# Optimization experiments

Hardware: AMD Instinct MI355X
Metric: run time of the kernel (lower is better)

## Reference

```python
import jax, jax.numpy as jnp
import numpy as np

N = 20000
F_IN = 500
HID = 64
CLS = 16
H = 4
K_KNN = 10
NEG_SLOPE = 0.2


def _edges(key, n_rand):
    # random edges plus self-loops (mirrors add_self_loops in the torch code)
    src = jax.random.randint(key, (n_rand,), 0, N)
    dst = jax.random.randint(jax.random.fold_in(key, 1), (n_rand,), 0, N)
    loops = jnp.arange(N)
    return jnp.stack([jnp.concatenate([src, loops]), jnp.concatenate([dst, loops])]).astype(jnp.int32)


def setup_inputs():
    key = jax.random.key(0)
    ks = jax.random.split(key, 40)
    inp = {}
    inp['x'] = jax.random.normal(ks[0], (N, F_IN), jnp.float32)
    inp['edge_index_1'] = _edges(ks[1], 16 * N)          # 1-hop graph, 340k edges
    inp['edge_index_2'] = _edges(ks[2], 32 * N)          # denser 2-hop graph, 660k edges
    knn_src = jnp.repeat(jnp.arange(N), K_KNN)
    knn_dst = jax.random.randint(ks[3], (K_KNN * N,), 0, N)
    inp['edge_index_knn'] = jnp.stack([knn_src, knn_dst]).astype(jnp.int32)

    def p(k, shape):
        return jax.random.normal(k, shape, jnp.float32) * 0.05

    dims = {1: (F_IN, HID), 2: (HID, CLS), 3: (F_IN, HID), 4: (HID, CLS), 5: (F_IN, HID), 6: (HID, CLS)}
    i = 4
    for j in range(1, 7):
        fi, fo = dims[j]
        inp[f'W{j}'] = p(ks[i], (fi, H, fo)); i += 1
        inp[f'as{j}'] = p(ks[i], (H, fo)); i += 1
        inp[f'ad{j}'] = p(ks[i], (H, fo)); i += 1
        inp[f'b{j}'] = jnp.zeros((fo,), jnp.float32)
    for j in range(1, 4):
        inp[f'lin{j}_w'] = p(ks[i], (CLS, CLS)); i += 1
        inp[f'lin{j}_b'] = jnp.zeros((CLS,), jnp.float32)
    inp['agg_w'] = p(ks[i], (CLS,))
    return inp


def gat_conv(x, ei, W, a_s, a_d, b):
    # PyG GATConv, concat=False (mean over heads). W: [F,H,D], a_s/a_d: [H,D], b: [D]
    src, dst = ei[0], ei[1]
    z = jnp.einsum('nf,fhd->nhd', x, W)                 # [N,H,D]
    e_src = jnp.sum(z * a_s, -1)                         # [N,H]
    e_dst = jnp.sum(z * a_d, -1)                         # [N,H]
    e = jax.nn.leaky_relu(e_src[src] + e_dst[dst], NEG_SLOPE)   # [E,H]
    m = jax.ops.segment_max(e, dst, num_segments=N)      # per-dst softmax (edge softmax)
    p = jnp.exp(e - m[dst])
    s = jax.ops.segment_sum(p, dst, num_segments=N)
    alpha = p / (s[dst] + 1e-16)                         # [E,H]
    out = jax.ops.segment_sum(alpha[:, :, None] * z[src], dst, num_segments=N)  # [N,H,D]
    return out.mean(1) + b


def reference(x, edge_index_1, edge_index_2, edge_index_knn,
              W1, as1, ad1, b1, W2, as2, ad2, b2,
              W3, as3, ad3, b3, W4, as4, ad4, b4,
              W5, as5, ad5, b5, W6, as6, ad6, b6,
              lin1_w, lin1_b, lin2_w, lin2_b, lin3_w, lin3_b, agg_w):
    # eval mode: dropout is a no-op
    h1 = jax.nn.relu(gat_conv(x, edge_index_1, W1, as1, ad1, b1))
    h1 = gat_conv(h1, edge_index_1, W2, as2, ad2, b2)
    h2 = jax.nn.relu(gat_conv(x, edge_index_2, W3, as3, ad3, b3))
    h2 = gat_conv(h2, edge_index_2, W4, as4, ad4, b4)
    h3 = jax.nn.relu(gat_conv(x, edge_index_knn, W5, as5, ad5, b5))
    h3 = gat_conv(h3, edge_index_knn, W6, as6, ad6, b6)

    a1 = jnp.tanh(h1 @ lin1_w + lin1_b) @ agg_w          # [N]
    a2 = jnp.tanh(h2 @ lin2_w + lin2_b) @ agg_w
    a3 = jnp.tanh(h3 @ lin3_w + lin3_b) @ agg_w
    a = jax.nn.softmax(jnp.stack([a1, a2, a3], axis=1), axis=1)  # [N,3]
    h = a[:, 0:1] * h1 + a[:, 1:2] * h2 + a[:, 2:3] * h3
    return jax.nn.log_softmax(h, axis=1)
```

## Files before the change

### kernel.cpp

```cpp
#include <hip/hip_runtime.h>
#include <hip/hip_bf16.h>
#include <math.h>

#define N_NODES 20000
#define MP      20096
#define FIN     500
#define KP      512
#define NBUCK   157

typedef unsigned short u16;
typedef unsigned char  u8;
typedef __attribute__((ext_vector_type(8))) short   short8;
typedef __attribute__((ext_vector_type(2))) unsigned uv2;
typedef __attribute__((ext_vector_type(2))) float   f32x2;
typedef __attribute__((ext_vector_type(4))) float   f32x4;

__device__ __forceinline__ float b2f(u16 u){
  union { unsigned int i; float f; } v; v.i = ((unsigned int)u) << 16; return v.f;
}
__device__ __forceinline__ u16 f2b(float f){
  __hip_bfloat16 h = __float2bfloat16(f);
  return *reinterpret_cast<u16*>(&h);
}
__device__ __forceinline__ float lrelu(float x){ return x >= 0.f ? x : 0.2f * x; }
__device__ __forceinline__ float ldp(const void* p, int i, int bf){
  return bf ? b2f(((const u16*)p)[i]) : ((const float*)p)[i];
}
__device__ __forceinline__ u8 f2fp8(float f){
  return (u8)(__builtin_amdgcn_cvt_pk_fp8_f32(f, 0.f, 0, false) & 0xff);
}
template<bool HI>
__device__ __forceinline__ f32x2 fp8pair(unsigned w){
  return __builtin_amdgcn_cvt_pk_f32_fp8((int)w, HI);
}
__device__ __forceinline__ void gll16(const u16* g, u16* l){
  __builtin_amdgcn_global_load_lds(
      (const __attribute__((address_space(1))) unsigned int*)g,
      (__attribute__((address_space(3))) unsigned int*)l, 16, 0, 0);
}

__global__ void detect_dtype_kernel(const unsigned int* __restrict__ xw, int nwords,
                                    int* __restrict__ flag){
  __shared__ int cnt;
  if (threadIdx.x == 0) cnt = 0;
  __syncthreads();
  int c = 0;
  for (int i = threadIdx.x; i < nwords; i += 256){
    unsigned e = (xw[i] >> 7) & 0xFF;
    if (e >= 0x70 && e <= 0x8F) c++;
  }
  atomicAdd(&cnt, c);
  __syncthreads();
  if (threadIdx.x == 0) *flag = (cnt * 2 > nwords) ? 1 : 0;
}

#define CHA 8192
__global__ __launch_bounds__(256) void prep_kernel(
    const void* __restrict__ x, u16* __restrict__ xp,
    const void* Wb0, const void* Wb1, const void* Wb2,
    const void* Ws0, const void* Ws1, const void* Ws2,
    u16* ob0, u16* ob1, u16* ob2, u16* os0, u16* os1, u16* os2,
    const int* s0, const int* s1, const int* s2,
    const int* d0, const int* d1, const int* d2,
    int E0, int E1, int E2, int S0, int S1, int S2, int EB,
    int* __restrict__ bucketCur, unsigned* p0, unsigned* p1, unsigned* p2,
    const int* __restrict__ flag){
  __shared__ int hb[NBUCK];
  __shared__ int hbase[NBUCK];
  int bf = *flag;
  if (blockIdx.y == 0){
    int t = blockIdx.x * 256 + threadIdx.x;
    if (t >= MP * 64) return;
    int row = t >> 6;
    int j0  = (t & 63) * 8;
    short8 v;
#pragma unroll
    for (int j = 0; j < 8; ++j){
      int k = j0 + j;
      u16 val = 0;
      if (row < N_NODES && k < FIN)
        val = bf ? ((const u16*)x)[(size_t)row * FIN + k]
                 : f2b(((const float*)x)[(size_t)row * FIN + k]);
      v[j] = (short)val;
    }
    *(short8*)(xp + (size_t)row * KP + j0) = v;
  } else if (blockIdx.y == 1){
    int xb = blockIdx.x;
    if (xb >= 6 * 512) return;
    int which = xb >> 9;
    int t = (xb & 511) * 256 + threadIdx.x;
    if (which < 3){
      if (t >= 256 * KP) return;
      const void* W = which == 0 ? Wb0 : (which == 1 ? Wb1 : Wb2);
      u16* O = which == 0 ? ob0 : (which == 1 ? ob1 : ob2);
      int n = t / KP, k = t % KP;
      u16 val = 0;
      if (k < FIN)
        val = bf ? ((const u16*)W)[(size_t)k * 256 + n]
                 : f2b(((const float*)W)[(size_t)k * 256 + n]);
      O[t] = val;
    } else {
      if (t >= 64 * 64) return;
      const void* W = which == 3 ? Ws0 : (which == 4 ? Ws1 : Ws2);
      u16* O = which == 3 ? os0 : (which == 4 ? os1 : os2);
      int n = t / 64, k = t % 64;
      O[t] = bf ? ((const u16*)W)[(size_t)k * 64 + n]
                : f2b(((const float*)W)[(size_t)k * 64 + n]);
    }
  } else {
    int sblk = blockIdx.x;
    if (sblk >= 3 * EB) return;
    int g = sblk / EB;
    const int* src = g == 0 ? s0 : (g == 1 ? s1 : s2);
    const int* dst = g == 0 ? d0 : (g == 1 ? d1 : d2);
    unsigned* pairs = g == 0 ? p0 : (g == 1 ? p1 : p2);
    int E = g == 0 ? E0 : (g == 1 ? E1 : E2);
    int S = g == 0 ? S0 : (g == 1 ? S1 : S2);
    int base = (sblk % EB) * CHA;
    if (base >= E) return;
    for (int i = threadIdx.x; i < NBUCK; i += 256) hb[i] = 0;
    __syncthreads();
    int rk[CHA / 256];
#pragma unroll
    for (int i = 0; i < CHA / 256; ++i){
      int e = base + i * 256 + threadIdx.x;
      rk[i] = 0;
      if (e < E) rk[i] = atomicAdd(&hb[dst[e] >> 7], 1);
    }
    __syncthreads();
    for (int i = threadIdx.x; i < NBUCK; i += 256)
      hbase[i] = atomicAdd(&bucketCur[g * NBUCK + i], hb[i]);
    __syncthreads();
#pragma unroll
    for (int i = 0; i < CHA / 256; ++i){
      int e = base + i * 256 + threadIdx.x;
      if (e < E){
        int d = dst[e];
        int b = d >> 7;
        int pos = hbase[b] + rk[i];
        if (pos < S)
          pairs[(size_t)b * S + pos] = ((unsigned)src[e] << 7) | (unsigned)(d & 127);
      }
    }
  }
}

__global__ __launch_bounds__(256) void csr_finalize_kernel(
    const unsigned* p0, const unsigned* p1, const unsigned* p2,
    int S0, int S1, int S2,
    const int* __restrict__ bucketCur,
    int* e0, int* e1, int* e2,
    int2* __restrict__ metaB){
  int g = blockIdx.y;
  const unsigned* pairs = g == 0 ? p0 : (g == 1 ? p1 : p2);
  int* esrc = g == 0 ? e0 : (g == 1 ? e1 : e2);
  int S = g == 0 ? S0 : (g == 1 ? S1 : S2);
  int2* meta = metaB + (size_t)g * MP;
  int b = blockIdx.x;
  int nb = bucketCur[g * NBUCK + b];
  if (nb > S) nb = S;
  const unsigned* pb = pairs + (size_t)b * S;
  int* eb = esrc + (size_t)b * S;
  __shared__ int cnt[128];
  __shared__ int loff[128];
  __shared__ int cur[128];
  if (threadIdx.x < 128) cnt[threadIdx.x] = 0;
  __syncthreads();
  for (int i = threadIdx.x; i < nb; i += 256)
    atomicAdd(&cnt[pb[i] & 127], 1);
  __syncthreads();
  if (threadIdx.x == 0){
    int run = 0;
    for (int k = 0; k < 128; ++k){ loff[k] = run; run += cnt[k]; }
  }
  __syncthreads();
  if (threadIdx.x < 128){
    cur[threadIdx.x] = loff[threadIdx.x];
    int d = b * 128 + threadIdx.x;
    if (d < N_NODES){
      int2 m; m.x = b * S + loff[threadIdx.x]; m.y = cnt[threadIdx.x];
      meta[d] = m;
    }
  }
  __syncthreads();
  for (int i = threadIdx.x; i < nb; i += 256){
    unsigned u = pb[i];
    int slot = atomicAdd(&cur[u & 127], 1);
    eb[slot] = (int)(u >> 7);
  }
}

__global__ __launch_bounds__(256) void gemm_big_kernel(const u16* __restrict__ A,
    const u16* B0, const u16* B1, const u16* B2,
    u8* C0, u8* C1, u8* C2,
    const void* as0, const void* as1, const void* as2,
    const void* ad0, const void* ad1, const void* ad2,
    float* __restrict__ esB, float* __restrict__ edB,
    const int* __restrict__ flag, int M){
  int g = blockIdx.z;
  const u16* BT = g == 0 ? B0 : (g == 1 ? B1 : B2);
  u8* C = g == 0 ? C0 : (g == 1 ? C1 : C2);
  const void* as_ = g == 0 ? as0 : (g == 1 ? as1 : as2);
  const void* ad_ = g == 0 ? ad0 : (g == 1 ? ad1 : ad2);
  float* es = esB + (size_t)g * N_NODES * 4;
  float* ed = edB + (size_t)g * N_NODES * 4;
  __shared__ alignas(16) u16 As[128 * 64];
  __shared__ alignas(16) u16 Bs[128 * 64];
  const int K = KP, Nn = 256;
  int t = threadIdx.x, lane = t & 63, w = t >> 6;
  int m0 = blockIdx.y * 128, n0 = blockIdx.x * 128;
  int mw = (w >> 1) * 64, nw = (w & 1) * 64;
  f32x4 acc[4][4] = {};
  for (int k0 = 0; k0 < K; k0 += 64){
    __syncthreads();
#pragma unroll
    for (int i = 0; i < 4; ++i){
      int c = i * 256 + w * 64 + lane;
      int row = c >> 3, kk = (c & 7) * 8;
      gll16(A  + (size_t)(m0 + row) * K + k0 + kk, As + (size_t)(i * 256 + w * 64) * 8);
      gll16(BT + (size_t)(n0 + row) * K + k0 + kk, Bs + (size_t)(i * 256 + w * 64) * 8);
    }
    __syncthreads();
#pragma unroll
    for (int ks = 0; ks < 2; ++ks){
      short8 af[4], bfr[4];
#pragma unroll
      for (int mi = 0; mi < 4; ++mi)
        af[mi] = *(const short8*)(As + (size_t)(mw + mi * 16 + (lane & 15)) * 64 + ks * 32 + (lane >> 4) * 8);
#pragma unroll
      for (int ni = 0; ni < 4; ++ni)
        bfr[ni] = *(const short8*)(Bs + (size_t)(nw + ni * 16 + (lane & 15)) * 64 + ks * 32 + (lane >> 4) * 8);
#pragma unroll
      for (int mi = 0; mi < 4; ++mi)
#pragma unroll
        for (int ni = 0; ni < 4; ++ni)
          acc[mi][ni] = __builtin_amdgcn_mfma_f32_16x16x32_bf16(af[mi], bfr[ni], acc[mi][ni], 0, 0, 0);
    }
  }
  int bf = *flag;
#pragma unroll
  for (int mi = 0; mi < 4; ++mi)
#pragma unroll
    for (int ni = 0; ni < 4; ++ni)
#pragma unroll
      for (int r = 0; r < 4; ++r){
        int row = m0 + mw + mi * 16 + (lane >> 4) * 4 + r;
        int col = n0 + nw + ni * 16 + (lane & 15);
        if (row < M) C[(size_t)row * Nn + col] = f2fp8(acc[mi][ni][r]);
      }
  {
    int h = (n0 + nw) >> 6;
    float asv[4], adv[4];
#pragma unroll
    for (int ni = 0; ni < 4; ++ni){
      int col = n0 + nw + ni * 16 + (lane & 15);
      asv[ni] = ldp(as_, col, bf);
      adv[ni] = ldp(ad_, col, bf);
    }
#pragma unroll
    for (int mi = 0; mi < 4; ++mi)
#pragma unroll
      for (int r = 0; r < 4; ++r){
        float ps = 0.f, pd2 = 0.f;
#pragma unroll
        for (int ni = 0; ni < 4; ++ni){
          ps  += acc[mi][ni][r] * asv[ni];
          pd2 += acc[mi][ni][r] * adv[ni];
        }
#pragma unroll
        for (int m2 = 1; m2 < 16; m2 <<= 1){
          ps  += __shfl_xor(ps, m2);
          pd2 += __shfl_xor(pd2, m2);
        }
        int row = m0 + mw + mi * 16 + (lane >> 4) * 4 + r;
        if ((lane & 15) == 0 && row < M){
          atomicAdd(es + (size_t)row * 4 + h, ps);
          atomicAdd(ed + (size_t)row * 4 + h, pd2);
        }
      }
  }
}

__global__ __launch_bounds__(256) void gemm_small_kernel(
    const u16* A0, const u16* A1, const u16* A2,
    const u16* B0, const u16* B1, const u16* B2,
    u8* C0, u8* C1, u8* C2,
    const void* as0, const void* as1, const void* as2,
    const void* ad0, const void* ad1, const void* ad2,
    float* __restrict__ esB, float* __restrict__ edB,
    const int* __restrict__ flag, int M){
  int g = blockIdx.y;
  const u16* A  = g == 0 ? A0 : (g == 1 ? A1 : A2);
  const u16* BT = g == 0 ? B0 : (g == 1 ? B1 : B2);
  u8* C = g == 0 ? C0 : (g == 1 ? C1 : C2);
  const void* as_ = g == 0 ? as0 : (g == 1 ? as1 : as2);
  const void* ad_ = g == 0 ? ad0 : (g == 1 ? ad1 : ad2);
  float* es = esB + (size_t)g * N_NODES * 4;
  float* ed = edB + (size_t)g * N_NODES * 4;
  __shared__ alignas(16) u16 As[64 * 64];
  __shared__ alignas(16) u16 Bs[64 * 64];
  int t = threadIdx.x, lane = t & 63, w = t >> 6;
  int m0 = blockIdx.x * 64;
#pragma unroll
  for (int i = 0; i < 2; ++i){
    int c = i * 256 + w * 64 + lane;
    int row = c >> 3, kk = (c & 7) * 8;
    gll16(A  + (size_t)(m0 + row) * 64 + kk, As + (size_t)(i * 256 + w * 64) * 8);
    gll16(BT + (size_t)row * 64 + kk,        Bs + (size_t)(i * 256 + w * 64) * 8);
  }
  __syncthreads();
  f32x4 acc[4] = {};
  int mw = w * 16;
#pragma unroll
  for (int ks = 0; ks < 2; ++ks){
    short8 af = *(const short8*)(As + (size_t)(mw + (lane & 15)) * 64 + ks * 32 + (lane >> 4) * 8);
#pragma unroll
    for (int ni = 0; ni < 4; ++ni){
      short8 bv = *(const short8*)(Bs + (size_t)(ni * 16 + (lane & 15)) * 64 + ks * 32 + (lane >> 4) * 8);
      acc[ni] = __builtin_amdgcn_mfma_f32_16x16x32_bf16(af, bv, acc[ni], 0, 0, 0);
    }
  }
  int bf = *flag;
#pragma unroll
  for (int ni = 0; ni < 4; ++ni)
#pragma unroll
    for (int r = 0; r < 4; ++r){
      int row = m0 + mw + (lane >> 4) * 4 + r;
      int col = ni * 16 + (lane & 15);
      if (row < M) C[(size_t)row * 64 + col] = f2fp8(acc[ni][r]);
    }
  {
    float asv[4], adv[4];
#pragma unroll
    for (int ni = 0; ni < 4; ++ni){
      int col = ni * 16 + (lane & 15);
      asv[ni] = ldp(as_, col, bf);
      adv[ni] = ldp(ad_, col, bf);
    }
#pragma unroll
    for (int r = 0; r < 4; ++r){
      float ps[4], pd2[4];
#pragma unroll
      for (int ni = 0; ni < 4; ++ni){ ps[ni] = acc[ni][r] * asv[ni]; pd2[ni] = acc[ni][r] * adv[ni]; }
#pragma unroll
      for (int m2 = 1; m2 < 16; m2 <<= 1)
#pragma unroll
        for (int ni = 0; ni < 4; ++ni){
          ps[ni]  += __shfl_xor(ps[ni], m2);
          pd2[ni] += __shfl_xor(pd2[ni], m2);
        }
      int row = m0 + mw + (lane >> 4) * 4 + r;
      if ((lane & 15) == 0 && row < M){
#pragma unroll
        for (int ni = 0; ni < 4; ++ni){
          es[(size_t)row * 4 + ni] = ps[ni];
          ed[(size_t)row * 4 + ni] = pd2[ni];
        }
      }
    }
  }
}

template<int DT, bool RELU, bool BF16OUT, int PIPE>
__global__ __launch_bounds__(256) void gat_agg5_kernel(
    const u8* z0, const u8* z1, const u8* z2,
    const float* __restrict__ esB, const float* __restrict__ edB,
    const int2* __restrict__ metaB,
    const int* e0p, const int* e1p, const int* e2p,
    const void* b0, const void* b1, const void* b2,
    void* o0, void* o1, void* o2,
    const int* __restrict__ flag){
  int g = blockIdx.y;
  const u8* z = g == 0 ? z0 : (g == 1 ? z1 : z2);
  const int* esrc = g == 0 ? e0p : (g == 1 ? e1p : e2p);
  const void* bias = g == 0 ? b0 : (g == 1 ? b1 : b2);
  void* out = g == 0 ? o0 : (g == 1 ? o1 : o2);
  const float* es = esB + (size_t)g * N_NODES * 4;
  const float* ed = edB + (size_t)g * N_NODES * 4;
  const int2* meta = metaB + (size_t)g * MP;
  int bf = *flag;

  int d = (blockIdx.x * 256 + threadIdx.x) >> 6;
  int lane = threadIdx.x & 63;
  if (d >= N_NODES) return;
  constexpr int LPG = DT / 8;
  constexpr int G   = 64 / LPG;
  constexpr int HD  = DT / 4;
  int grp = lane / LPG;
  int li  = lane % LPG;
  int c0  = li * 8;
  int h   = c0 / HD;

  int2 md = meta[d];
  int deg = md.y;
  const int* ep = esrc + md.x;
  float edh = ed[(unsigned)d * 4 + h];

  float acc[8] = {0,0,0,0,0,0,0,0};
  float sacc = 0.f;

  int steps = (deg + PIPE * G - 1) / (PIPE * G);
  for (int tb = 0; tb < steps; ++tb){
    int e0 = tb * PIPE * G + grp;
    int s[PIPE]; float q[PIPE]; uv2 v[PIPE]; bool val[PIPE];
#pragma unroll
    for (int i = 0; i < PIPE; ++i){
      int e = e0 + i * G;
      val[i] = e < deg;
      int sl = ep[e];
      s[i] = val[i] ? sl : 0;
    }
#pragma unroll
    for (int i = 0; i < PIPE; ++i) q[i] = es[(unsigned)s[i] * 4 + h];
#pragma unroll
    for (int i = 0; i < PIPE; ++i) v[i] = *(const uv2*)(z + (unsigned)s[i] * DT + c0);
#pragma unroll
    for (int i = 0; i < PIPE; ++i){
      float p = val[i] ? __expf(lrelu(q[i] + edh)) : 0.f;
      sacc += p;
      f32x2 a0 = fp8pair<false>(v[i][0]), a1 = fp8pair<true>(v[i][0]);
      f32x2 a2 = fp8pair<false>(v[i][1]), a3 = fp8pair<true>(v[i][1]);
      acc[0] = fmaf(p, a0.x, acc[0]); acc[1] = fmaf(p, a0.y, acc[1]);
      acc[2] = fmaf(p, a1.x, acc[2]); acc[3] = fmaf(p, a1.y, acc[3]);
      acc[4] = fmaf(p, a2.x, acc[4]); acc[5] = fmaf(p, a2.y, acc[5]);
      acc[6] = fmaf(p, a3.x, acc[6]); acc[7] = fmaf(p, a3.y, acc[7]);
    }
  }

#pragma unroll
  for (int m = LPG; m < 64; m <<= 1){
    sacc += __shfl_xor(sacc, m);
#pragma unroll
    for (int j = 0; j < 8; ++j) acc[j] += __shfl_xor(acc[j], m);
  }
  float inv = 1.f / (sacc + 1e-16f);
  float v8[8];
#pragma unroll
  for (int j = 0; j < 8; ++j) v8[j] = acc[j] * inv;
#pragma unroll
  for (int m = HD / 8; m < LPG; m <<= 1)
#pragma unroll
    for (int j = 0; j < 8; ++j) v8[j] += __shfl_xor(v8[j], m);

  if (lane < HD / 8){
    if constexpr (BF16OUT){
      short8 ov;
#pragma unroll
      for (int j = 0; j < 8; ++j){
        float o = v8[j] * 0.25f + ldp(bias, lane * 8 + j, bf);
        if (RELU) o = fmaxf(o, 0.f);
        ov[j] = (short)f2b(o);
      }
      *(short8*)((u16*)out + (size_t)d * HD + lane * 8) = ov;
    } else {
      float o[8];
#pragma unroll
      for (int j = 0; j < 8; ++j){
        o[j] = v8[j] * 0.25f + ldp(bias, lane * 8 + j, bf);
        if (RELU) o[j] = fmaxf(o[j], 0.f);
      }
      float* op = (float*)out + (size_t)d * HD + lane * 8;
      *(float4*)op = make_float4(o[0], o[1], o[2], o[3]);
      *(float4*)(op + 4) = make_float4(o[4], o[5], o[6], o[7]);
    }
  }
}

__global__ __launch_bounds__(256) void final_combine_kernel(
    const float* __restrict__ h1, const float* __restrict__ h2, const float* __restrict__ h3,
    const void* l1w, const void* l1b, const void* l2w, const void* l2b,
    const void* l3w, const void* l3b, const void* aggw,
    void* __restrict__ outv, int n, const int* __restrict__ flag){
  __shared__ float Lw[3][16][16];
  __shared__ float Lb[3][16];
  __shared__ float Ag[16];
  int t = threadIdx.x;
  int bf = *flag;
  {
    const void* ws[3] = { l1w, l2w, l3w };
    for (int g = 0; g < 3; ++g) Lw[g][t / 16][t % 16] = ldp(ws[g], t, bf);
    if (t < 16){
      Lb[0][t] = ldp(l1b, t, bf); Lb[1][t] = ldp(l2b, t, bf); Lb[2][t] = ldp(l3b, t, bf);
      Ag[t] = ldp(aggw, t, bf);
    }
  }
  __syncthreads();
  int node = blockIdx.x * 256 + t;
  if (node >= n) return;
  const float* hp[3] = { h1, h2, h3 };
  float hv[3][16];
  float a[3];
  for (int g = 0; g < 3; ++g){
    const float4* h4 = (const float4*)(hp[g] + (size_t)node * 16);
#pragma unroll
    for (int q = 0; q < 4; ++q){
      float4 f = h4[q];
      hv[g][q * 4 + 0] = f.x; hv[g][q * 4 + 1] = f.y;
      hv[g][q * 4 + 2] = f.z; hv[g][q * 4 + 3] = f.w;
    }
    float dot = 0.f;
#pragma unroll
    for (int j = 0; j < 16; ++j){
      float acc2 = Lb[g][j];
#pragma unroll
      for (int i = 0; i < 16; ++i) acc2 += hv[g][i] * Lw[g][i][j];
      dot += tanhf(acc2) * Ag[j];
    }
    a[g] = dot;
  }
  float am = fmaxf(a[0], fmaxf(a[1], a[2]));
  float e0 = __expf(a[0] - am), e1 = __expf(a[1] - am), e2 = __expf(a[2] - am);
  float einv = 1.f / (e0 + e1 + e2);
  float w0 = e0 * einv, w1 = e1 * einv, w2 = e2 * einv;
  float hh[16];
  float hmax = -INFINITY;
#pragma unroll
  for (int i = 0; i < 16; ++i){
    hh[i] = w0 * hv[0][i] + w1 * hv[1][i] + w2 * hv[2][i];
    hmax = fmaxf(hmax, hh[i]);
  }
  float se = 0.f;
#pragma unroll
  for (int i = 0; i < 16; ++i) se += __expf(hh[i] - hmax);
  float ls = hmax + logf(se);
#pragma unroll
  for (int i = 0; i < 16; ++i){
    float o = hh[i] - ls;
    if (bf) ((__hip_bfloat16*)outv)[(size_t)node * 16 + i] = __float2bfloat16(o);
    else    ((float*)outv)[(size_t)node * 16 + i] = o;
  }
}

extern "C" void kernel_launch(void* const* d_in, const int* in_sizes, int n_in,
                              void* d_out, int out_size, void* d_ws, size_t ws_size,
                              hipStream_t stream){
  const void* x = d_in[0];
  const int* ei[3] = { (const int*)d_in[1], (const int*)d_in[2], (const int*)d_in[3] };
  int E[3] = { in_sizes[1] / 2, in_sizes[2] / 2, in_sizes[3] / 2 };
  int Emax = E[0] > E[1] ? E[0] : E[1]; if (E[2] > Emax) Emax = E[2];
  int EB = (Emax + CHA - 1) / CHA;
  int S[3];
  for (int g = 0; g < 3; ++g){
    long s = ((long)E[g] * 27 / 20) / NBUCK + 64;
    s &= ~63L; if (s > 8192) s = 8192;
    S[g] = (int)s;
  }
  const void *W[6], *as_[6], *ad_[6], *bb[6];
  for (int j = 0; j < 6; ++j){
    W[j]   = d_in[4 + 4 * j];
    as_[j] = d_in[5 + 4 * j];
    ad_[j] = d_in[6 + 4 * j];
    bb[j]  = d_in[7 + 4 * j];
  }
  const void* l1w = d_in[28]; const void* l1b = d_in[29];
  const void* l2w = d_in[30]; const void* l2b = d_in[31];
  const void* l3w = d_in[32]; const void* l3b = d_in[33];
  const void* agg = d_in[34];

  char* p = (char*)d_ws;
  auto alloc = [&](size_t bytes) -> void* {
    void* r = (void*)p;
    p += (bytes + 255) & ~(size_t)255;
    return r;
  };
  int* dflag = (int*)alloc(256);
  u16* xp = (u16*)alloc((size_t)MP * KP * 2);
  u16* hmid[3]; for (int g = 0; g < 3; ++g) hmid[g] = xp + (size_t)g * MP * 64;
  u16* wtb[3]; for (int g = 0; g < 3; ++g) wtb[g] = (u16*)alloc((size_t)256 * KP * 2);
  u16* wts[3]; for (int g = 0; g < 3; ++g) wts[g] = (u16*)alloc((size_t)64 * 64 * 2);
  u8* zf[3];   for (int g = 0; g < 3; ++g) zf[g]  = (u8*)alloc((size_t)N_NODES * 256 + 256);
  float* hbr[3]; for (int g = 0; g < 3; ++g) hbr[g] = (float*)alloc((size_t)N_NODES * 16 * 4);
  float* esB = (float*)alloc((size_t)3 * N_NODES * 4 * 4);
  float* edB = (float*)alloc((size_t)3 * N_NODES * 4 * 4);
  int* bucketCur = (int*)alloc((size_t)3 * NBUCK * 4);
  size_t zero_span = (char*)(bucketCur + 3 * NBUCK) - (char*)esB;
  int2* metaB    = (int2*)alloc((size_t)3 * MP * 8);
  int* esrc[3];
  for (int g = 0; g < 3; ++g) esrc[g] = (int*)alloc(((size_t)NBUCK * S[g] + 256) * 4);
  unsigned* pairs[3];
  for (int g = 0; g < 3; ++g) pairs[g] = (unsigned*)alloc(((size_t)NBUCK * S[g] + 256) * 4);

  const int* s0 = ei[0];          const int* s1 = ei[1];          const int* s2 = ei[2];
  const int* d0 = ei[0] + E[0];   const int* d1 = ei[1] + E[1];   const int* d2 = ei[2] + E[2];

  (void)hipMemsetAsync(esB, 0, zero_span, stream);
  detect_dtype_kernel<<<1, 256, 0, stream>>>((const unsigned int*)x, 16384, dflag);
  prep_kernel<<<dim3((MP * 64 + 255) / 256, 3), 256, 0, stream>>>(
      x, xp, W[0], W[2], W[4], W[1], W[3], W[5],
      wtb[0], wtb[1], wtb[2], wts[0], wts[1], wts[2],
      s0, s1, s2, d0, d1, d2, E[0], E[1], E[2], S[0], S[1], S[2], EB,
      bucketCur, pairs[0], pairs[1], pairs[2], dflag);
  csr_finalize_kernel<<<dim3(NBUCK, 3), 256, 0, stream>>>(
      pairs[0], pairs[1], pairs[2], S[0], S[1], S[2], bucketCur,
      esrc[0], esrc[1], esrc[2], metaB);

  const int convGrid = (N_NODES + 3) / 4;

  gemm_big_kernel<<<dim3(2, MP / 128, 3), 256, 0, stream>>>(
      xp, wtb[0], wtb[1], wtb[2], zf[0], zf[1], zf[2],
      as_[0], as_[2], as_[4], ad_[0], ad_[2], ad_[4], esB, edB, dflag, N_NODES);
  gat_agg5_kernel<256, true, true, 6><<<dim3(convGrid, 3), 256, 0, stream>>>(
      zf[0], zf[1], zf[2], esB, edB, metaB, esrc[0], esrc[1], esrc[2],
      bb[0], bb[2], bb[4], (void*)hmid[0], (void*)hmid[1], (void*)hmid[2], dflag);

  gemm_small_kernel<<<dim3(MP / 64, 3), 256, 0, stream>>>(
      hmid[0], hmid[1], hmid[2], wts[0], wts[1], wts[2], zf[0], zf[1], zf[2],
      as_[1], as_[3], as_[5], ad_[1], ad_[3], ad_[5], esB, edB, dflag, N_NODES);
  gat_agg5_kernel<64, false, false, 4><<<dim3(convGrid, 3), 256, 0, stream>>>(
      zf[0], zf[1], zf[2], esB, edB, metaB, esrc[0], esrc[1], esrc[2],
      bb[1], bb[3], bb[5], (void*)hbr[0], (void*)hbr[1], (void*)hbr[2], dflag);

  final_combine_kernel<<<(N_NODES + 255) / 256, 256, 0, stream>>>(
      hbr[0], hbr[1], hbr[2], l1w, l1b, l2w, l2b, l3w, l3b, agg,
      d_out, N_NODES, dflag);
}
```

Before: 395.3 us.

## XOR-swizzle GEMM LDS tiles and replace score atomics with plain stores

Applies an XOR swizzle (slot ^ row&7) to the 16-byte chunks written into and read from shared memory in both GEMM kernels, so MFMA fragment loads spread across LDS banks instead of conflicting. Each row/head attention score now has a single writer, so the atomicAdds into es/ed become direct stores. This lets the memset shrink to only the bucket counters. The risk is correctness if any es/ed element still gets more than one contributor.

```diff
diff --git a/kernel.cpp b/kernel.cpp
--- a/kernel.cpp
+++ b/kernel.cpp
@@ -216,7 +216,8 @@
 #pragma unroll
     for (int i = 0; i < 4; ++i){
       int c = i * 256 + w * 64 + lane;
-      int row = c >> 3, kk = (c & 7) * 8;
+      int row = c >> 3, slot = c & 7;
+      int kk = ((slot ^ (row & 7))) * 8;
       gll16(A  + (size_t)(m0 + row) * K + k0 + kk, As + (size_t)(i * 256 + w * 64) * 8);
       gll16(BT + (size_t)(n0 + row) * K + k0 + kk, Bs + (size_t)(i * 256 + w * 64) * 8);
     }
@@ -225,11 +226,17 @@
     for (int ks = 0; ks < 2; ++ks){
       short8 af[4], bfr[4];
 #pragma unroll
-      for (int mi = 0; mi < 4; ++mi)
-        af[mi] = *(const short8*)(As + (size_t)(mw + mi * 16 + (lane & 15)) * 64 + ks * 32 + (lane >> 4) * 8);
-#pragma unroll
-      for (int ni = 0; ni < 4; ++ni)
-        bfr[ni] = *(const short8*)(Bs + (size_t)(nw + ni * 16 + (lane & 15)) * 64 + ks * 32 + (lane >> 4) * 8);
+      for (int mi = 0; mi < 4; ++mi){
+        int row = mw + mi * 16 + (lane & 15);
+        int sl = (ks * 4 + (lane >> 4)) ^ (row & 7);
+        af[mi] = *(const short8*)(As + (size_t)row * 64 + sl * 8);
+      }
+#pragma unroll
+      for (int ni = 0; ni < 4; ++ni){
+        int row = nw + ni * 16 + (lane & 15);
+        int sl = (ks * 4 + (lane >> 4)) ^ (row & 7);
+        bfr[ni] = *(const short8*)(Bs + (size_t)row * 64 + sl * 8);
+      }
 #pragma unroll
       for (int mi = 0; mi < 4; ++mi)
 #pragma unroll
@@ -274,8 +281,8 @@
         }
         int row = m0 + mw + mi * 16 + (lane >> 4) * 4 + r;
         if ((lane & 15) == 0 && row < M){
-          atomicAdd(es + (size_t)row * 4 + h, ps);
-          atomicAdd(ed + (size_t)row * 4 + h, pd2);
+          es[(size_t)row * 4 + h] = ps;
+          ed[(size_t)row * 4 + h] = pd2;
         }
       }
   }
@@ -304,7 +311,8 @@
 #pragma unroll
   for (int i = 0; i < 2; ++i){
     int c = i * 256 + w * 64 + lane;
-    int row = c >> 3, kk = (c & 7) * 8;
+    int row = c >> 3, slot = c & 7;
+    int kk = ((slot ^ (row & 7))) * 8;
     gll16(A  + (size_t)(m0 + row) * 64 + kk, As + (size_t)(i * 256 + w * 64) * 8);
     gll16(BT + (size_t)row * 64 + kk,        Bs + (size_t)(i * 256 + w * 64) * 8);
   }
@@ -313,10 +321,14 @@
   int mw = w * 16;
 #pragma unroll
   for (int ks = 0; ks < 2; ++ks){
-    short8 af = *(const short8*)(As + (size_t)(mw + (lane & 15)) * 64 + ks * 32 + (lane >> 4) * 8);
+    int rowa = mw + (lane & 15);
+    int sla = (ks * 4 + (lane >> 4)) ^ (rowa & 7);
+    short8 af = *(const short8*)(As + (size_t)rowa * 64 + sla * 8);
 #pragma unroll
     for (int ni = 0; ni < 4; ++ni){
-      short8 bv = *(const short8*)(Bs + (size_t)(ni * 16 + (lane & 15)) * 64 + ks * 32 + (lane >> 4) * 8);
+      int rowb = ni * 16 + (lane & 15);
+      int slb = (ks * 4 + (lane >> 4)) ^ (rowb & 7);
+      short8 bv = *(const short8*)(Bs + (size_t)rowb * 64 + slb * 8);
       acc[ni] = __builtin_amdgcn_mfma_f32_16x16x32_bf16(af, bv, acc[ni], 0, 0, 0);
     }
   }
@@ -573,7 +585,6 @@
   float* esB = (float*)alloc((size_t)3 * N_NODES * 4 * 4);
   float* edB = (float*)alloc((size_t)3 * N_NODES * 4 * 4);
   int* bucketCur = (int*)alloc((size_t)3 * NBUCK * 4);
-  size_t zero_span = (char*)(bucketCur + 3 * NBUCK) - (char*)esB;
   int2* metaB    = (int2*)alloc((size_t)3 * MP * 8);
   int* esrc[3];
   for (int g = 0; g < 3; ++g) esrc[g] = (int*)alloc(((size_t)NBUCK * S[g] + 256) * 4);
@@ -583,7 +594,7 @@
   const int* s0 = ei[0];          const int* s1 = ei[1];          const int* s2 = ei[2];
   const int* d0 = ei[0] + E[0];   const int* d1 = ei[1] + E[1];   const int* d2 = ei[2] + E[2];
 
-  (void)hipMemsetAsync(esB, 0, zero_span, stream);
+  (void)hipMemsetAsync(bucketCur, 0, (size_t)3 * NBUCK * 4, stream);
   detect_dtype_kernel<<<1, 256, 0, stream>>>((const unsigned int*)x, 16384, dflag);
   prep_kernel<<<dim3((MP * 64 + 255) / 256, 3), 256, 0, stream>>>(
       x, xp, W[0], W[2], W[4], W[1], W[3], W[5],
```

Result: faster. 378.8 us (-4.2%).
